# Performance work log

Hardware: AMD Instinct MI355X
Metric: run time of the kernel (lower is better)

The kernel has to match this reference:

```python
import jax, jax.numpy as jnp
import numpy as np
import math

MAX_K = 8
MAX_LEN = 128
ITER = 3
GAMMA = 2
NEG = -2.0**16 + 1.0  # mask fill value from torch code


def _squash(x):
    # NOTE: faithful to source: norm taken over axis=1 (capsule axis), keepdim
    sq = jnp.sum(x * x, axis=1, keepdims=True)
    return sq / (1.0 + sq) / jnp.sqrt(sq + 1e-9) * x


def _routing(low, B_mat, S):
    # low: [B, n, d] mailbox; B_mat: [1, MAX_K, MAX_LEN]; S: [d, d]
    n = low.shape[1]
    K_c = max(1, min(MAX_K, int(math.log2(n))))  # static per edge type
    low_new = jnp.einsum('bnd,de->bne', low, S)  # loop-invariant in torch too
    B_c = B_mat[:, :K_c, :]
    mask = jnp.arange(MAX_LEN) < n  # padded-neighbor mask
    high = None
    for _ in range(ITER):
        logits = jnp.where(mask, B_c, NEG)              # [1,K_c,L]
        W = jax.nn.softmax(logits, axis=-1)[:, :, :n]   # weights identical over batch
        high = _squash(jnp.einsum('xkn,bnd->bkd', W, low_new))
        delta = jnp.einsum('bkd,bnd->kn', high, low_new)  # batch-summed agreement
        B_c = B_c.at[0, :, :n].add(delta)  # padded cols get zero delta (zeros in low)
    high = jnp.pad(high, ((0, 0), (0, MAX_K - K_c), (0, 0)))
    # torch B_matrix_c aliases B_matrix; write slice back so next etype sees updates
    return high, B_mat.at[:, :K_c, :].set(B_c)


def setup_inputs() -> dict:
    key = jax.random.key(0)
    ks = jax.random.split(key, 12)
    d = 64
    n_user, n_rev, n_tag, n_rev_dst = 10000, 30000, 40000, 8000
    f = lambda k, s: jax.random.normal(k, s, dtype=jnp.float32)
    return {
        'review_embed': f(ks[0], (n_rev, d)),
        'tag_embed': f(ks[1], (n_tag, d)),
        'idx_urt': jax.random.randint(ks[2], (n_user, 64), 0, n_rev, dtype=jnp.int32),
        'idx_uqt': jax.random.randint(ks[3], (n_user, 32), 0, n_tag, dtype=jnp.int32),
        'idx_uprt': jax.random.randint(ks[4], (n_user, 50), 0, n_rev, dtype=jnp.int32),
        'idx_rht': jax.random.randint(ks[5], (n_rev_dst, 20), 0, n_tag, dtype=jnp.int32),
        'B_matrix': f(ks[6], (1, MAX_K, MAX_LEN)),
        'S_matrix': f(ks[7], (d, d)),
        'M1': f(ks[8], (d, d)),
        'M2': f(ks[9], (d, 1)),
    }


def reference(review_embed, tag_embed, idx_urt, idx_uqt, idx_uprt, idx_rht,
              B_matrix, S_matrix, M1, M2):
    # capsule routing per edge type, B_matrix threaded sequentially (torch aliasing)
    h_urt, B_matrix = _routing(review_embed[idx_urt], B_matrix, S_matrix)
    h_uqt, B_matrix = _routing(tag_embed[idx_uqt], B_matrix, S_matrix)
    h_uprt, B_matrix = _routing(review_embed[idx_uprt], B_matrix, S_matrix)
    all_u = jnp.concatenate([h_urt, h_uqt, h_uprt], axis=1)  # [B, 3*MAX_K, d]
    s = jnp.einsum('bkd,do->bko', jnp.tanh(jnp.einsum('bkd,de->bke', all_u, M1)), M2)[..., 0]
    s = s ** GAMMA
    att = jax.nn.softmax(s, axis=1)                # [B, 3*MAX_K]
    user_out = jnp.einsum('bk,bkd->bd', att, all_u)
    review_out = jnp.mean(tag_embed[idx_rht], axis=1)  # flag==2 mean reduce (r_h_t)
    return user_out, review_out
```

## Files before the change

### kernel.cpp

```cpp
#include <hip/hip_runtime.h>

#define NU 10000
#define NREV_DST 8000
#define MAIN_BLOCKS 512
#define TW (MAIN_BLOCKS * 4)
#define UPW ((NU + TW - 1) / TW)


template <int N, int K>
__global__ __launch_bounds__(256) void main_iter(
    const float* __restrict__ emb, const int* __restrict__ idx,
    const float* __restrict__ Sg, const float* __restrict__ Wg,
    float* __restrict__ delta_acc, float* __restrict__ allu,
    int slot0, int write_high, int write_delta)
{
    constexpr int NC = (N + 31) / 32;
    constexpr int P  = NC * 32;

    __shared__ float s_S[64 * 65];
    __shared__ float s_emb[4][32 * 65];
    __shared__ float s_g[4][K * 64];
    __shared__ float s_h[4][K * 64];

    const int tid  = threadIdx.x;
    const int w    = tid >> 6;
    const int lane = tid & 63;
    const int gw   = blockIdx.x * 4 + w;

    for (int i = tid; i < 64 * 64; i += 256) {
        s_S[(i >> 6) * 65 + (i & 63)] = Sg[i];
    }
    __syncthreads();

    float dreg[NC][K];
#pragma unroll
    for (int c = 0; c < NC; ++c)
#pragma unroll
        for (int k = 0; k < K; ++k) dreg[c][k] = 0.f;

    auto stage = [&](int u, int c, int m) {
        const int npass = (m + 3) >> 2;
        for (int p = 0; p < npass; ++p) {
            const int r = p * 4 + (lane >> 4);
            if (r < m) {
                const int row = idx[u * N + c * 32 + r];
                const float4 v =
                    *reinterpret_cast<const float4*>(emb + (size_t)row * 64 + (lane & 15) * 4);
                float* dst = &s_emb[w][r * 65 + (lane & 15) * 4];
                dst[0] = v.x; dst[1] = v.y; dst[2] = v.z; dst[3] = v.w;
            }
        }
    };

    for (int it = 0; it < UPW; ++it) {
        const int u = gw + it * TW;
        if (u < NU) {
            float g[K];
#pragma unroll
            for (int k = 0; k < K; ++k) g[k] = 0.f;
#pragma unroll
            for (int c = 0; c < NC; ++c) {
                const int m = (N - c * 32 < 32) ? (N - c * 32) : 32;
                stage(u, c, m);
                for (int r = 0; r < m; ++r) {
                    const float ev = s_emb[w][r * 65 + lane];
#pragma unroll
                    for (int k = 0; k < K; ++k)
                        g[k] = fmaf(Wg[k * 64 + c * 32 + r], ev, g[k]);
                }
            }
#pragma unroll
            for (int k = 0; k < K; ++k) s_g[w][k * 64 + lane] = g[k];
            float raw[K];
#pragma unroll
            for (int k = 0; k < K; ++k) raw[k] = 0.f;
            for (int e = 0; e < 64; ++e) {
                const float sv = s_S[e * 65 + lane];
#pragma unroll
                for (int k = 0; k < K; ++k) raw[k] = fmaf(s_g[w][k * 64 + e], sv, raw[k]);
            }
            float sq = 0.f;
#pragma unroll
            for (int k = 0; k < K; ++k) sq = fmaf(raw[k], raw[k], sq);
            const float f = (sq / (1.0f + sq)) / sqrtf(sq + 1e-9f);
            float hi[K];
#pragma unroll
            for (int k = 0; k < K; ++k) hi[k] = f * raw[k];
            if (write_high) {
#pragma unroll
                for (int k = 0; k < K; ++k)
                    allu[(size_t)u * 1024 + (slot0 + k) * 64 + lane] = hi[k];
            }
            if (write_delta) {
#pragma unroll
                for (int k = 0; k < K; ++k) s_h[w][k * 64 + lane] = hi[k];
                float hs[K];
#pragma unroll
                for (int k = 0; k < K; ++k) hs[k] = 0.f;
                for (int d = 0; d < 64; ++d) {
                    const float sv = s_S[lane * 65 + d];
#pragma unroll
                    for (int k = 0; k < K; ++k) hs[k] = fmaf(s_h[w][k * 64 + d], sv, hs[k]);
                }
#pragma unroll
                for (int k = 0; k < K; ++k) s_g[w][k * 64 + lane] = hs[k];
                const int nl = lane & 31, h = lane >> 5;
#pragma unroll
                for (int cc = NC - 1; cc >= 0; --cc) {
                    const int m = (N - cc * 32 < 32) ? (N - cc * 32) : 32;
                    if (cc != NC - 1) stage(u, cc, m);
                    if (nl < m) {
                        for (int eh = 0; eh < 32; ++eh) {
                            const int e = h * 32 + eh;
                            const float ev = s_emb[w][nl * 65 + e];
#pragma unroll
                            for (int k = 0; k < K; ++k)
                                dreg[cc][k] = fmaf(ev, s_g[w][k * 64 + e], dreg[cc][k]);
                        }
                    }
                }
            }
        }
    }

    if (write_delta) {
        __syncthreads();
        float* red = &s_emb[w][0];
        const int nl = lane & 31;
#pragma unroll
        for (int cc = 0; cc < NC; ++cc) {
#pragma unroll
            for (int k = 0; k < K; ++k) {
                const float v = dreg[cc][k] + __shfl_xor(dreg[cc][k], 32, 64);
                if (lane < 32) red[k * P + cc * 32 + nl] = v;
            }
        }
        __syncthreads();
        for (int t = tid; t < K * P; t += 256) {
            const float s = s_emb[0][t] + s_emb[1][t] + s_emb[2][t] + s_emb[3][t];
            const int k = t / P, n = t % P;
            atomicAdd(&delta_acc[k * 64 + n], s);
        }
    }
}

__global__ __launch_bounds__(1024) void update_kernel(
    float* __restrict__ Bstate, float* __restrict__ delta_acc,
    const float* __restrict__ Bin, float* __restrict__ Wout,
    int init, int Kc, int nc, int Kn, int nn)
{
    __shared__ float sB[1024];
    const int t = threadIdx.x;
    float b = init ? Bin[t] : Bstate[t];
    const int k = t >> 7, n = t & 127;
    float d = 0.f;
    if (!init && k < Kc && n < nc) d = delta_acc[k * 64 + n];
    __syncthreads();
    if (t < 512) delta_acc[t] = 0.f;
    b += d;
    Bstate[t] = b;
    sB[t] = b;
    __syncthreads();
    const int wv = t >> 6, lane = t & 63;
    if (wv < Kn) {
        float v = (lane < nn) ? sB[wv * 128 + lane] : -3.4e38f;
        float m = v;
#pragma unroll
        for (int off = 32; off >= 1; off >>= 1) m = fmaxf(m, __shfl_xor(m, off, 64));
        const float e = (lane < nn) ? expf(v - m) : 0.f;
        float s = e;
#pragma unroll
        for (int off = 32; off >= 1; off >>= 1) s += __shfl_xor(s, off, 64);
        Wout[wv * 64 + lane] = e / s;
    }
}

__global__ __launch_bounds__(256) void attn_kernel(
    const float* __restrict__ allu, const float* __restrict__ M1g,
    const float* __restrict__ M2g, float* __restrict__ out)
{
    __shared__ float sM1[64 * 65];
    __shared__ float sU[4][16 * 64];
    const int tid = threadIdx.x, w = tid >> 6, lane = tid & 63;
    for (int i = tid; i < 4096; i += 256)
        sM1[(i >> 6) * 65 + (i & 63)] = M1g[i];
    __syncthreads();
    const int u = blockIdx.x * 4 + w;
    if (u >= NU) return;
    for (int i = 0; i < 16; ++i)
        sU[w][i * 64 + lane] = allu[(size_t)u * 1024 + i * 64 + lane];
    const float m2 = M2g[lane];
    float acc[16];
#pragma unroll
    for (int i = 0; i < 16; ++i) acc[i] = 0.f;
    for (int d = 0; d < 64; ++d) {
        const float m1v = sM1[d * 65 + lane];
#pragma unroll
        for (int i = 0; i < 16; ++i) acc[i] = fmaf(sU[w][i * 64 + d], m1v, acc[i]);
    }
    float s2[16];
#pragma unroll
    for (int i = 0; i < 16; ++i) {
        float c = tanhf(acc[i]) * m2;
#pragma unroll
        for (int off = 32; off >= 1; off >>= 1) c += __shfl_xor(c, off, 64);
        s2[i] = c * c;
    }
    float mx = 0.f;
#pragma unroll
    for (int i = 0; i < 16; ++i) mx = fmaxf(mx, s2[i]);
    float den = 8.f * expf(-mx);
    float att[16];
#pragma unroll
    for (int i = 0; i < 16; ++i) { att[i] = expf(s2[i] - mx); den += att[i]; }
    const float inv = 1.0f / den;
    float o = 0.f;
#pragma unroll
    for (int i = 0; i < 16; ++i) o = fmaf(att[i] * inv, sU[w][i * 64 + lane], o);
    out[(size_t)u * 64 + lane] = o;
}

__global__ __launch_bounds__(256) void review_kernel(
    const float* __restrict__ tag, const int* __restrict__ idx, float* __restrict__ out)
{
    const int tid = threadIdx.x, w = tid >> 6, lane = tid & 63;
    const int r = blockIdx.x * 4 + w;
    if (r >= NREV_DST) return;
    float acc = 0.f;
    for (int j = 0; j < 20; ++j) {
        const int t = idx[r * 20 + j];
        acc += tag[(size_t)t * 64 + lane];
    }
    out[(size_t)r * 64 + lane] = acc / 20.0f;
}

extern "C" void kernel_launch(void* const* d_in, const int* in_sizes, int n_in,
                              void* d_out, int out_size, void* d_ws, size_t ws_size,
                              hipStream_t stream)
{
    const float* review_embed = (const float*)d_in[0];
    const float* tag_embed    = (const float*)d_in[1];
    const int*   idx_urt      = (const int*)d_in[2];
    const int*   idx_uqt      = (const int*)d_in[3];
    const int*   idx_uprt     = (const int*)d_in[4];
    const int*   idx_rht      = (const int*)d_in[5];
    const float* B_in         = (const float*)d_in[6];
    const float* S_g          = (const float*)d_in[7];
    const float* M1           = (const float*)d_in[8];
    const float* M2           = (const float*)d_in[9];

    float* ws     = (float*)d_ws;
    float* Bstate = ws;
    float* delta  = ws + 1024;
    float* Wbuf   = ws + 1536;
    float* allu   = ws + 2048;
    float* out    = (float*)d_out;

    const dim3 mg(MAIN_BLOCKS), mb(256);
    const dim3 one(1), ub(1024);

    hipLaunchKernelGGL(update_kernel, one, ub, 0, stream,
                       Bstate, delta, B_in, Wbuf, 1, 0, 0, 6, 64);

    for (int itr = 0; itr < 3; ++itr) {
        hipLaunchKernelGGL((main_iter<64, 6>), mg, mb, 0, stream,
                           review_embed, idx_urt, S_g, Wbuf, delta, allu,
                           0, (itr == 2) ? 1 : 0, 1);
        const int Kn = (itr == 2) ? 5 : 6;
        const int nn = (itr == 2) ? 32 : 64;
        hipLaunchKernelGGL(update_kernel, one, ub, 0, stream,
                           Bstate, delta, B_in, Wbuf, 0, 6, 64, Kn, nn);
    }
    for (int itr = 0; itr < 3; ++itr) {
        hipLaunchKernelGGL((main_iter<32, 5>), mg, mb, 0, stream,
                           tag_embed, idx_uqt, S_g, Wbuf, delta, allu,
                           6, (itr == 2) ? 1 : 0, 1);
        const int nn = (itr == 2) ? 50 : 32;
        hipLaunchKernelGGL(update_kernel, one, ub, 0, stream,
                           Bstate, delta, B_in, Wbuf, 0, 5, 32, 5, nn);
    }
    for (int itr = 0; itr < 3; ++itr) {
        const int last = (itr == 2);
        hipLaunchKernelGGL((main_iter<50, 5>), mg, mb, 0, stream,
                           review_embed, idx_uprt, S_g, Wbuf, delta, allu,
                           11, last, last ? 0 : 1);
        if (!last)
            hipLaunchKernelGGL(update_kernel, one, ub, 0, stream,
                               Bstate, delta, B_in, Wbuf, 0, 5, 50, 5, 50);
    }

    hipLaunchKernelGGL(attn_kernel, dim3((NU + 3) / 4), mb, 0, stream, allu, M1, M2, out);
    hipLaunchKernelGGL(review_kernel, dim3((NREV_DST + 3) / 4), mb, 0, stream,
                       tag_embed, idx_rht, out + (size_t)NU * 64);
}
```

Before: 660.0 us.

## Replace shared-memory matvecs with readlane broadcasts and direct gathered delta loads

Drops the shared-memory copies of S, g and h and computes the S and S^T matvecs with cross-lane readlane broadcasts, reading S from global/cache. The delta pass now has each lane load its own neighbor row directly as float4 instead of restaging tiles, and per-lane delta accumulators shrink to K registers. The grid doubles to 1024 blocks and launch bounds request 4 blocks per CU to raise occupancy. The trade-offs are many scalar readlane operations in place of LDS reads, and extra uncoalesced global gathers in the delta phase.

New measurement: 895.7 us. 1.36x slower.

```diff
diff --git a/kernel.cpp b/kernel.cpp
--- a/kernel.cpp
+++ b/kernel.cpp
@@ -2,122 +2,117 @@
 
 #define NU 10000
 #define NREV_DST 8000
-#define MAIN_BLOCKS 512
-#define TW (MAIN_BLOCKS * 4)
-#define UPW ((NU + TW - 1) / TW)
-
+#define MAIN_GRID 1024
+
+
+__device__ __forceinline__ float rlane(float v, int l) {
+    return __int_as_float(__builtin_amdgcn_readlane(__float_as_int(v), l));
+}
 
 template <int N, int K>
-__global__ __launch_bounds__(256) void main_iter(
+__global__ __launch_bounds__(256, 4) void main_iter(
     const float* __restrict__ emb, const int* __restrict__ idx,
     const float* __restrict__ Sg, const float* __restrict__ Wg,
     float* __restrict__ delta_acc, float* __restrict__ allu,
     int slot0, int write_high, int write_delta)
 {
     constexpr int NC = (N + 31) / 32;
-    constexpr int P  = NC * 32;
-
-    __shared__ float s_S[64 * 65];
     __shared__ float s_emb[4][32 * 65];
-    __shared__ float s_g[4][K * 64];
-    __shared__ float s_h[4][K * 64];
 
     const int tid  = threadIdx.x;
     const int w    = tid >> 6;
     const int lane = tid & 63;
+    const int tw   = gridDim.x * 4;
     const int gw   = blockIdx.x * 4 + w;
 
-    for (int i = tid; i < 64 * 64; i += 256) {
-        s_S[(i >> 6) * 65 + (i & 63)] = Sg[i];
-    }
-    __syncthreads();
-
-    float dreg[NC][K];
-#pragma unroll
-    for (int c = 0; c < NC; ++c)
-#pragma unroll
-        for (int k = 0; k < K; ++k) dreg[c][k] = 0.f;
-
-    auto stage = [&](int u, int c, int m) {
-        const int npass = (m + 3) >> 2;
-        for (int p = 0; p < npass; ++p) {
-            const int r = p * 4 + (lane >> 4);
-            if (r < m) {
-                const int row = idx[u * N + c * 32 + r];
-                const float4 v =
-                    *reinterpret_cast<const float4*>(emb + (size_t)row * 64 + (lane & 15) * 4);
-                float* dst = &s_emb[w][r * 65 + (lane & 15) * 4];
-                dst[0] = v.x; dst[1] = v.y; dst[2] = v.z; dst[3] = v.w;
-            }
-        }
-    };
-
-    for (int it = 0; it < UPW; ++it) {
-        const int u = gw + it * TW;
-        if (u < NU) {
-            float g[K];
-#pragma unroll
-            for (int k = 0; k < K; ++k) g[k] = 0.f;
-#pragma unroll
-            for (int c = 0; c < NC; ++c) {
-                const int m = (N - c * 32 < 32) ? (N - c * 32) : 32;
-                stage(u, c, m);
-                for (int r = 0; r < m; ++r) {
-                    const float ev = s_emb[w][r * 65 + lane];
-#pragma unroll
-                    for (int k = 0; k < K; ++k)
-                        g[k] = fmaf(Wg[k * 64 + c * 32 + r], ev, g[k]);
-                }
-            }
-#pragma unroll
-            for (int k = 0; k < K; ++k) s_g[w][k * 64 + lane] = g[k];
-            float raw[K];
-#pragma unroll
-            for (int k = 0; k < K; ++k) raw[k] = 0.f;
-            for (int e = 0; e < 64; ++e) {
-                const float sv = s_S[e * 65 + lane];
-#pragma unroll
-                for (int k = 0; k < K; ++k) raw[k] = fmaf(s_g[w][k * 64 + e], sv, raw[k]);
-            }
-            float sq = 0.f;
-#pragma unroll
-            for (int k = 0; k < K; ++k) sq = fmaf(raw[k], raw[k], sq);
-            const float f = (sq / (1.0f + sq)) / sqrtf(sq + 1e-9f);
-            float hi[K];
-#pragma unroll
-            for (int k = 0; k < K; ++k) hi[k] = f * raw[k];
-            if (write_high) {
-#pragma unroll
-                for (int k = 0; k < K; ++k)
-                    allu[(size_t)u * 1024 + (slot0 + k) * 64 + lane] = hi[k];
-            }
-            if (write_delta) {
-#pragma unroll
-                for (int k = 0; k < K; ++k) s_h[w][k * 64 + lane] = hi[k];
-                float hs[K];
-#pragma unroll
-                for (int k = 0; k < K; ++k) hs[k] = 0.f;
-                for (int d = 0; d < 64; ++d) {
-                    const float sv = s_S[lane * 65 + d];
-#pragma unroll
-                    for (int k = 0; k < K; ++k) hs[k] = fmaf(s_h[w][k * 64 + d], sv, hs[k]);
-                }
-#pragma unroll
-                for (int k = 0; k < K; ++k) s_g[w][k * 64 + lane] = hs[k];
-                const int nl = lane & 31, h = lane >> 5;
-#pragma unroll
-                for (int cc = NC - 1; cc >= 0; --cc) {
-                    const int m = (N - cc * 32 < 32) ? (N - cc * 32) : 32;
-                    if (cc != NC - 1) stage(u, cc, m);
-                    if (nl < m) {
-                        for (int eh = 0; eh < 32; ++eh) {
-                            const int e = h * 32 + eh;
-                            const float ev = s_emb[w][nl * 65 + e];
-#pragma unroll
-                            for (int k = 0; k < K; ++k)
-                                dreg[cc][k] = fmaf(ev, s_g[w][k * 64 + e], dreg[cc][k]);
-                        }
-                    }
+    float dreg[K];
+#pragma unroll
+    for (int k = 0; k < K; ++k) dreg[k] = 0.f;
+
+    for (int u = gw; u < NU; u += tw) {
+        float g[K];
+#pragma unroll
+        for (int k = 0; k < K; ++k) g[k] = 0.f;
+
+        for (int c = 0; c < NC; ++c) {
+            const int m = (N - c * 32 < 32) ? (N - c * 32) : 32;
+            const int npass = (m + 3) >> 2;
+            for (int p = 0; p < npass; ++p) {
+                const int r = p * 4 + (lane >> 4);
+                if (r < m) {
+                    const int row = idx[u * N + c * 32 + r];
+                    const float4 v = *reinterpret_cast<const float4*>(
+                        emb + (size_t)row * 64 + (lane & 15) * 4);
+                    float* dst = &s_emb[w][r * 65 + (lane & 15) * 4];
+                    dst[0] = v.x; dst[1] = v.y; dst[2] = v.z; dst[3] = v.w;
+                }
+            }
+            for (int r = 0; r < m; r += 2) {
+                const float e0 = s_emb[w][r * 65 + lane];
+                const float e1 = s_emb[w][(r + 1) * 65 + lane];
+#pragma unroll
+                for (int k = 0; k < K; ++k) {
+                    g[k] = fmaf(Wg[k * 64 + c * 32 + r],     e0, g[k]);
+                    g[k] = fmaf(Wg[k * 64 + c * 32 + r + 1], e1, g[k]);
+                }
+            }
+        }
+
+        float raw[K];
+#pragma unroll
+        for (int k = 0; k < K; ++k) raw[k] = 0.f;
+        for (int e0 = 0; e0 < 64; e0 += 4) {
+            float sv0 = Sg[(e0 + 0) * 64 + lane];
+            float sv1 = Sg[(e0 + 1) * 64 + lane];
+            float sv2 = Sg[(e0 + 2) * 64 + lane];
+            float sv3 = Sg[(e0 + 3) * 64 + lane];
+#pragma unroll
+            for (int k = 0; k < K; ++k) {
+                raw[k] = fmaf(rlane(g[k], e0 + 0), sv0, raw[k]);
+                raw[k] = fmaf(rlane(g[k], e0 + 1), sv1, raw[k]);
+                raw[k] = fmaf(rlane(g[k], e0 + 2), sv2, raw[k]);
+                raw[k] = fmaf(rlane(g[k], e0 + 3), sv3, raw[k]);
+            }
+        }
+
+        float sq = 0.f;
+#pragma unroll
+        for (int k = 0; k < K; ++k) sq = fmaf(raw[k], raw[k], sq);
+        const float f = (sq / (1.0f + sq)) / sqrtf(sq + 1e-9f);
+        float hi[K];
+#pragma unroll
+        for (int k = 0; k < K; ++k) hi[k] = f * raw[k];
+        if (write_high) {
+#pragma unroll
+            for (int k = 0; k < K; ++k)
+                allu[(size_t)u * 1024 + (slot0 + k) * 64 + lane] = hi[k];
+        }
+
+        if (write_delta) {
+            float hs[K];
+#pragma unroll
+            for (int k = 0; k < K; ++k) hs[k] = 0.f;
+            for (int d0 = 0; d0 < 64; d0 += 4) {
+                const float4 sr = *reinterpret_cast<const float4*>(Sg + lane * 64 + d0);
+#pragma unroll
+                for (int k = 0; k < K; ++k) {
+                    hs[k] = fmaf(rlane(hi[k], d0 + 0), sr.x, hs[k]);
+                    hs[k] = fmaf(rlane(hi[k], d0 + 1), sr.y, hs[k]);
+                    hs[k] = fmaf(rlane(hi[k], d0 + 2), sr.z, hs[k]);
+                    hs[k] = fmaf(rlane(hi[k], d0 + 3), sr.w, hs[k]);
+                }
+            }
+            const int nclamp = (lane < N) ? lane : 0;
+            const int row = idx[u * N + nclamp];
+            const float* ep = emb + (size_t)row * 64;
+            for (int e0 = 0; e0 < 64; e0 += 4) {
+                const float4 ev = *reinterpret_cast<const float4*>(ep + e0);
+#pragma unroll
+                for (int k = 0; k < K; ++k) {
+                    dreg[k] = fmaf(ev.x, rlane(hs[k], e0 + 0), dreg[k]);
+                    dreg[k] = fmaf(ev.y, rlane(hs[k], e0 + 1), dreg[k]);
+                    dreg[k] = fmaf(ev.z, rlane(hs[k], e0 + 2), dreg[k]);
+                    dreg[k] = fmaf(ev.w, rlane(hs[k], e0 + 3), dreg[k]);
                 }
             }
         }
@@ -125,21 +120,13 @@
 
     if (write_delta) {
         __syncthreads();
-        float* red = &s_emb[w][0];
-        const int nl = lane & 31;
-#pragma unroll
-        for (int cc = 0; cc < NC; ++cc) {
-#pragma unroll
-            for (int k = 0; k < K; ++k) {
-                const float v = dreg[cc][k] + __shfl_xor(dreg[cc][k], 32, 64);
-                if (lane < 32) red[k * P + cc * 32 + nl] = v;
-            }
-        }
+        float* sflat = &s_emb[0][0];
+#pragma unroll
+        for (int k = 0; k < K; ++k) sflat[(w * K + k) * 64 + lane] = dreg[k];
         __syncthreads();
-        for (int t = tid; t < K * P; t += 256) {
-            const float s = s_emb[0][t] + s_emb[1][t] + s_emb[2][t] + s_emb[3][t];
-            const int k = t / P, n = t % P;
-            atomicAdd(&delta_acc[k * 64 + n], s);
+        for (int t = tid; t < K * 64; t += 256) {
+            const float s = sflat[t] + sflat[K * 64 + t] + sflat[2 * K * 64 + t] + sflat[3 * K * 64 + t];
+            if ((t & 63) < N) atomicAdd(&delta_acc[t], s);
         }
     }
 }
@@ -256,7 +243,7 @@
     float* allu   = ws + 2048;
     float* out    = (float*)d_out;
 
-    const dim3 mg(MAIN_BLOCKS), mb(256);
+    const dim3 mg(MAIN_GRID), mb(256);
     const dim3 one(1), ub(1024);
 
     hipLaunchKernelGGL(update_kernel, one, ub, 0, stream,
```
